# Performance work log

Measured on AMD Instinct MI355X. Metric: run time of the kernel, lower is better.

Reference implementation:

```python
import jax, jax.numpy as jnp
import numpy as np

N = 50000
E = 800000
F = 128
HID = 128
C = 40
GAMMA = 0.1
EPS = 0.1


def gcn(x, theta, src, dst, n):
    # GCNConv (bias=False) with added self-loops and symmetric normalization.
    xw = x @ theta  # [N, d]
    ones = jnp.ones(src.shape[0], dtype=x.dtype)
    deg = jax.ops.segment_sum(ones, dst, num_segments=n) + 1.0  # in-degree incl. self loop
    dinv = jax.lax.rsqrt(deg)
    norm = dinv[src] * dinv[dst]            # [E]
    msg = xw[src] * norm[:, None]           # [E, d]  (dominant memory traffic)
    agg = jax.ops.segment_sum(msg, dst, num_segments=n)
    return agg + xw * (dinv * dinv)[:, None]  # self-loop contribution


def antisym_conv(x, W, bias, theta, src, dst, n):
    # PyG AntiSymmetricConv, num_iters=1, act=tanh, eps=0.1, gamma=0.1
    M = W - W.T - GAMMA * jnp.eye(W.shape[0], dtype=x.dtype)
    h = gcn(x, theta, src, dst, n)
    h = x @ M.T + h + bias
    return x + EPS * jnp.tanh(h)


def setup_inputs() -> dict:
    key = jax.random.key(0)
    ks = jax.random.split(key, 12)
    s = 0.05
    return {
        "x": jax.random.normal(ks[0], (N, F), dtype=jnp.float32),
        "edge_index": jax.random.randint(ks[1], (2, E), 0, N, dtype=jnp.int64)
        if jax.config.jax_enable_x64 else jax.random.randint(ks[1], (2, E), 0, N, dtype=jnp.int32),
        # AntiSymmetricConv 1 (num_features channels)
        "W1": jax.random.normal(ks[2], (F, F), dtype=jnp.float32) * s,
        "b1": jnp.zeros((F,), dtype=jnp.float32),
        "T1": jax.random.normal(ks[3], (F, F), dtype=jnp.float32) * s,
        # AntiSymmetricConv 2 (nhid channels)
        "W2": jax.random.normal(ks[4], (HID, HID), dtype=jnp.float32) * s,
        "b2": jnp.zeros((HID,), dtype=jnp.float32),
        "T2": jax.random.normal(ks[5], (HID, HID), dtype=jnp.float32) * s,
        # Linear layers (torch convention: weight [out, in])
        "lw1": jax.random.normal(ks[6], (HID, F), dtype=jnp.float32) * s,
        "lb1": jnp.zeros((HID,), dtype=jnp.float32),
        "lw2": jax.random.normal(ks[7], (C, HID), dtype=jnp.float32) * s,
        "lb2": jnp.zeros((C,), dtype=jnp.float32),
    }


def reference(x, edge_index, W1, b1, T1, W2, b2, T2, lw1, lb1, lw2, lb2):
    src, dst = edge_index[0], edge_index[1]
    n = x.shape[0]
    # eval mode: dropout is identity
    h = antisym_conv(x, W1, b1, T1, src, dst, n)
    h = jax.nn.relu(h)
    h = h @ lw1.T + lb1
    h = jax.nn.relu(h)
    h = antisym_conv(h, W2, b2, T2, src, dst, n)
    h = jax.nn.relu(h)
    x1 = h
    logits = h @ lw2.T + lb2
    result = jax.nn.log_softmax(logits, axis=-1)
    return (result, x1)
```

## Files before the change

kernel.cpp:

```cpp
#include <hip/hip_runtime.h>
#include <hip/hip_bf16.h>
#include <math.h>

#define GAMMA_ 0.1f
#define EPS_ 0.1f
constexpr int BLK = 256;

typedef __attribute__((ext_vector_type(8))) short short8;
typedef __attribute__((ext_vector_type(4))) float f32x4;
typedef __attribute__((ext_vector_type(2))) float f32x2v;
typedef unsigned char u8;

__device__ inline float bflo(uint u) { union { uint i; float f; } v; v.i = u << 16; return v.f; }
__device__ inline float bfhi(uint u) { union { uint i; float f; } v; v.i = u & 0xffff0000u; return v.f; }
__device__ inline ushort f2bf(float f) {
  union { float f; uint i; } v; v.f = f;
  uint i = v.i;
  return (ushort)((i + 0x7fffu + ((i >> 16) & 1u)) >> 16);
}

#if __has_builtin(__builtin_amdgcn_cvt_pk_f32_fp8) && __has_builtin(__builtin_amdgcn_cvt_pk_fp8_f32)
#define HW_FP8 1
#endif

__device__ inline f32x2v fp8x2_dec_sw(uint raw) {
  f32x2v r;
#pragma unroll
  for (int i = 0; i < 2; ++i) {
    uint b = (raw >> (8 * i)) & 0xffu;
    uint em = b & 0x7fu;
    union { uint u; float f; } o;
    o.u = ((b & 0x80u) << 24) | (0x3C000000u + (em << 20));
    r[i] = (em >= 8u) ? o.f : 0.f;
  }
  return r;
}

__device__ inline f32x2v fp8x2_dec(uint raw) {
#ifdef HW_FP8
  return __builtin_amdgcn_cvt_pk_f32_fp8(raw, false);
#else
  return fp8x2_dec_sw(raw);
#endif
}

__device__ inline uint fp8enc1(float x) {
  union { float f; uint u; } v; v.f = x;
  uint s = (v.u >> 24) & 0x80u;
  uint a = v.u & 0x7fffffffu;
  if (a >= 0x43E00000u) return s | 0x7Eu;
  uint r = a + 0x7FFFFu + ((a >> 20) & 1u);
  if (r < 0x3D800000u) return s;
  return s | (((r - 0x3C000000u) >> 20) & 0x7fu);
}

template<bool HI>
__device__ inline uint fp8x2_enc(float f0, float f1, uint old) {
#ifdef HW_FP8
  return __builtin_amdgcn_cvt_pk_fp8_f32(f0, f1, old, HI);
#else
  uint p = fp8enc1(f0) | (fp8enc1(f1) << 8);
  return HI ? ((old & 0x0000ffffu) | (p << 16)) : ((old & 0xffff0000u) | p);
#endif
}

__global__ void k_count(const int* __restrict__ dst, int* cnt,
                        int* __restrict__ rank, int e) {
  int i = blockIdx.x * BLK + threadIdx.x;
  if (i < e) rank[i] = atomicAdd(&cnt[dst[i]], 1);
}

__global__ void k_scan1(const int* __restrict__ cnt, int* __restrict__ rowp,
                        int* __restrict__ bsum, int n) {
  __shared__ int s[BLK];
  int t = threadIdx.x;
  int i = blockIdx.x * BLK + t;
  int v = (i < n) ? cnt[i] : 0;
  s[t] = v; __syncthreads();
  for (int off = 1; off < BLK; off <<= 1) {
    int u = (t >= off) ? s[t - off] : 0;
    __syncthreads();
    s[t] += u;
    __syncthreads();
  }
  if (i < n) rowp[i] = s[t] - v;
  if (t == BLK - 1) bsum[blockIdx.x] = s[t];
}

__global__ void k_scan2(const int* __restrict__ bsum, int* __restrict__ boff, int nb) {
  __shared__ int s[BLK];
  int t = threadIdx.x;
  int v = (t < nb) ? bsum[t] : 0;
  s[t] = v; __syncthreads();
  for (int off = 1; off < BLK; off <<= 1) {
    int u = (t >= off) ? s[t - off] : 0;
    __syncthreads();
    s[t] += u;
    __syncthreads();
  }
  if (t < nb) boff[t] = s[t] - v;
}

__global__ void k_scan3(const int* __restrict__ boff, int* __restrict__ rowp,
                        const int* __restrict__ cnt, float* __restrict__ dinv,
                        int n, int e) {
  int i = blockIdx.x * BLK + threadIdx.x;
  if (i < n) {
    rowp[i] += boff[blockIdx.x];
    dinv[i] = rsqrtf((float)cnt[i] + 1.0f);
    if (i == 0) rowp[n] = e;
  }
}

__global__ void k_fill(const int* __restrict__ src, const int* __restrict__ dst,
                       const int* __restrict__ rowp, const int* __restrict__ rank,
                       int* __restrict__ csrc, int e) {
  int i = blockIdx.x * BLK + threadIdx.x;
  if (i < e) {
    int d = dst[i];
    csrc[rowp[d] + rank[i]] = src[i];
  }
}

__global__ void k_pack(const float* __restrict__ W1, const float* __restrict__ T1,
                       const float* __restrict__ W2, const float* __restrict__ T2,
                       const float* __restrict__ lw1, const float* __restrict__ lw2,
                       ushort* __restrict__ Bpk1, ushort* __restrict__ Bpk2,
                       ushort* __restrict__ Bpkl, ushort* __restrict__ Bpk2l) {
  int idx = blockIdx.x * BLK + threadIdx.x;
  if (idx < 65536) {
    int which = idx >> 15;
    int e = idx & 32767;
    int k = e >> 8, c = e & 255;
    const float* W = which ? W2 : W1;
    const float* T = which ? T2 : T1;
    float v;
    if (c < 128) {
      v = T[k * 128 + c];
    } else {
      int cc = c - 128;
      v = W[cc * 128 + k] - W[k * 128 + cc] - ((cc == k) ? GAMMA_ : 0.f);
    }
    int kt = k >> 5, q = (k >> 3) & 3, j = k & 7;
    ushort* B = which ? Bpk2 : Bpk1;
    B[(((kt * 4 + q) * 256 + c) << 3) + j] = f2bf(v);
  } else if (idx < 81920) {
    int e = idx - 65536;
    int k = e >> 7, c = e & 127;
    float v = lw1[c * 128 + k];
    int kt = k >> 5, q = (k >> 3) & 3, j = k & 7;
    Bpkl[(((kt * 4 + q) * 128 + c) << 3) + j] = f2bf(v);
  } else {
    int e = idx - 81920;
    if (e < 6144) {
      int k = e / 48, c = e - k * 48;
      float v = (c < 40) ? lw2[c * 128 + k] : 0.f;
      int kt = k >> 5, q = (k >> 3) & 3, j = k & 7;
      Bpk2l[(((kt * 4 + q) * 48 + c) << 3) + j] = f2bf(v);
    }
  }
}

template<bool FP32A>
__global__ __launch_bounds__(256) void k_mgemm(
    const void* __restrict__ Av, int nrows,
    const ushort* __restrict__ Bpk, const float* __restrict__ dinv,
    ushort* __restrict__ O1, u8* __restrict__ Oq) {
  __shared__ ushort S[64 * 256];
  const int t = threadIdx.x;
  const int w = t >> 6, l = t & 63;
  const int lr = l & 15, lq = l >> 4;
  const int r0 = blockIdx.x * 64;
#pragma unroll
  for (int it = 0; it < 4; ++it) {
    int chunk = it * 256 + t;
    int row = chunk >> 4, c16 = chunk & 15;
    int gr = min(r0 + row, nrows - 1);
    ushort* p = S + row * 128 + (c16 ^ (row & 7)) * 8;
    if (FP32A) {
      const float* A = (const float*)Av + (size_t)gr * 128 + c16 * 8;
      float4 v0 = *(const float4*)(A);
      float4 v1 = *(const float4*)(A + 4);
      ushort4 o0 = {f2bf(v0.x), f2bf(v0.y), f2bf(v0.z), f2bf(v0.w)};
      ushort4 o1 = {f2bf(v1.x), f2bf(v1.y), f2bf(v1.z), f2bf(v1.w)};
      *(ushort4*)(p) = o0;
      *(ushort4*)(p + 4) = o1;
    } else {
      const ushort* A = (const ushort*)Av + (size_t)gr * 128 + c16 * 8;
      *(uint4*)p = *(const uint4*)A;
    }
  }
  __syncthreads();
  f32x4 acc[4][4];
#pragma unroll
  for (int rt = 0; rt < 4; ++rt)
#pragma unroll
    for (int n = 0; n < 4; ++n) acc[rt][n] = f32x4{0.f, 0.f, 0.f, 0.f};
#pragma unroll
  for (int kt = 0; kt < 4; ++kt) {
    short8 af[4];
#pragma unroll
    for (int rt = 0; rt < 4; ++rt) {
      int row = rt * 16 + lr;
      af[rt] = *(const short8*)(S + row * 128 + ((kt * 4 + lq) ^ (row & 7)) * 8);
    }
    const ushort* bbase = Bpk + ((size_t)((kt * 4 + lq) * 256) + w * 64 + lr) * 8;
#pragma unroll
    for (int n = 0; n < 4; ++n) {
      short8 bf = *(const short8*)(bbase + n * 16 * 8);
#pragma unroll
      for (int rt = 0; rt < 4; ++rt)
        acc[rt][n] = __builtin_amdgcn_mfma_f32_16x16x32_bf16(af[rt], bf, acc[rt][n], 0, 0, 0);
    }
  }
  __syncthreads();
#pragma unroll
  for (int rt = 0; rt < 4; ++rt)
#pragma unroll
    for (int n = 0; n < 4; ++n)
#pragma unroll
      for (int r = 0; r < 4; ++r) {
        int row = rt * 16 + lq * 4 + r;
        int col = w * 64 + n * 16 + lr;
        int pcol = col ^ (((row >> 2) & 3) << 3);
        S[row * 256 + pcol] = f2bf(acc[rt][n][r]);
      }
  __syncthreads();
#pragma unroll
  for (int it = 0; it < 4; ++it) {
    int idx = it * 256 + t;
    int row = idx >> 4, c8 = idx & 15;
    if (r0 + row < nrows) {
      int pc = (16 + (c8 ^ ((row >> 2) & 3))) * 8;
      uint4 v = *(const uint4*)(S + row * 256 + pc);
      *(uint4*)(O1 + (size_t)(r0 + row) * 128 + c8 * 8) = v;
    }
  }
#pragma unroll
  for (int it = 0; it < 4; ++it) {
    int idx = it * 256 + t;
    int row = idx >> 4, c8 = idx & 15;
    if (r0 + row < nrows) {
      float di = dinv[r0 + row];
      int pc = (c8 ^ ((row >> 2) & 3)) * 8;
      const uint* p = (const uint*)(S + row * 256 + pc);
      uint u0 = p[0], u1 = p[1], u2 = p[2], u3 = p[3];
      uint lo = fp8x2_enc<false>(bflo(u0) * di, bfhi(u0) * di, 0u);
      lo = fp8x2_enc<true>(bflo(u1) * di, bfhi(u1) * di, lo);
      uint hi = fp8x2_enc<false>(bflo(u2) * di, bfhi(u2) * di, 0u);
      hi = fp8x2_enc<true>(bflo(u3) * di, bfhi(u3) * di, hi);
      uint2 ov = { lo, hi };
      *(uint2*)(Oq + (size_t)(r0 + row) * 128 + c8 * 8) = ov;
    }
  }
}

__device__ inline void gather_node(const u8* __restrict__ xq,
                                   const int* __restrict__ csrc,
                                   int e0, int e1, int l, int node,
                                   float& a0, float& a1) {
  uint su = *(const ushort*)(xq + (size_t)node * 128 + 2 * l);
  f32x2v sf = fp8x2_dec(su);
  a0 = sf[0]; a1 = sf[1];
  int e = e0;
  for (; e + 15 < e1; e += 16) {
    int s[16];
#pragma unroll
    for (int u = 0; u < 16; ++u) s[u] = csrc[e + u];
    uint g[16];
#pragma unroll
    for (int u = 0; u < 16; ++u)
      g[u] = *(const ushort*)(xq + (size_t)s[u] * 128 + 2 * l);
#pragma unroll
    for (int u = 0; u < 16; ++u) {
      f32x2v f = fp8x2_dec(g[u]);
      a0 += f[0]; a1 += f[1];
    }
  }
  if (e + 7 < e1) {
    int s[8];
#pragma unroll
    for (int u = 0; u < 8; ++u) s[u] = csrc[e + u];
    uint g[8];
#pragma unroll
    for (int u = 0; u < 8; ++u)
      g[u] = *(const ushort*)(xq + (size_t)s[u] * 128 + 2 * l);
#pragma unroll
    for (int u = 0; u < 8; ++u) {
      f32x2v f = fp8x2_dec(g[u]);
      a0 += f[0]; a1 += f[1];
    }
    e += 8;
  }
  if (e + 3 < e1) {
    int s[4];
#pragma unroll
    for (int u = 0; u < 4; ++u) s[u] = csrc[e + u];
    uint g[4];
#pragma unroll
    for (int u = 0; u < 4; ++u)
      g[u] = *(const ushort*)(xq + (size_t)s[u] * 128 + 2 * l);
#pragma unroll
    for (int u = 0; u < 4; ++u) {
      f32x2v f = fp8x2_dec(g[u]);
      a0 += f[0]; a1 += f[1];
    }
    e += 4;
  }
  for (; e < e1; ++e) {
    uint g0 = *(const ushort*)(xq + (size_t)csrc[e] * 128 + 2 * l);
    f32x2v f = fp8x2_dec(g0);
    a0 += f[0]; a1 += f[1];
  }
}

__global__ __launch_bounds__(512) void k_aggl(
    const u8* __restrict__ xq, const ushort* __restrict__ xmb,
    const float* __restrict__ xinf, const float* __restrict__ dinv,
    const int* __restrict__ rowp, const int* __restrict__ csrc,
    const float* __restrict__ bias, const ushort* __restrict__ Bpkl,
    const float* __restrict__ lb1, ushort* __restrict__ h2b, int n) {
  __shared__ ushort Hs[32 * 128];
  const int t = threadIdx.x;
  const int w = t >> 6, l = t & 63;
  const int lr = l & 15, lq = l >> 4;
  const int r0 = blockIdx.x * 32;
#pragma unroll
  for (int i = 0; i < 4; ++i) {
    int lrow = w * 4 + i;
    int node = r0 + lrow;
    float o0 = 0.f, o1 = 0.f;
    if (node < n) {
      float a0, a1;
      gather_node(xq, csrc, rowp[node], rowp[node + 1], l, node, a0, a1);
      float di = dinv[node];
      uint mu = *(const uint*)(xmb + (size_t)node * 128 + 2 * l);
      float h0 = a0 * di + bflo(mu) + bias[2 * l];
      float h1 = a1 * di + bfhi(mu) + bias[2 * l + 1];
      float2 xv = *(const float2*)(xinf + (size_t)node * 128 + 2 * l);
      o0 = fmaxf(xv.x + EPS_ * tanhf(h0), 0.f);
      o1 = fmaxf(xv.y + EPS_ * tanhf(h1), 0.f);
    }
    ushort2 o = { f2bf(o0), f2bf(o1) };
    *(ushort2*)(Hs + lrow * 128 + ((l >> 2) ^ (lrow & 7)) * 8 + (l & 3) * 2) = o;
  }
  __syncthreads();
  f32x4 acc[2];
  acc[0] = f32x4{0.f, 0.f, 0.f, 0.f};
  acc[1] = f32x4{0.f, 0.f, 0.f, 0.f};
#pragma unroll
  for (int kt = 0; kt < 4; ++kt) {
    short8 bf = *(const short8*)(Bpkl + ((size_t)((kt * 4 + lq) * 128) + w * 16 + lr) * 8);
#pragma unroll
    for (int rt = 0; rt < 2; ++rt) {
      int row = rt * 16 + lr;
      short8 af = *(const short8*)(Hs + row * 128 + ((kt * 4 + lq) ^ (row & 7)) * 8);
      acc[rt] = __builtin_amdgcn_mfma_f32_16x16x32_bf16(af, bf, acc[rt], 0, 0, 0);
    }
  }
  int col = w * 16 + lr;
  float bv = lb1[col];
#pragma unroll
  for (int rt = 0; rt < 2; ++rt)
#pragma unroll
    for (int r = 0; r < 4; ++r) {
      int row = rt * 16 + lq * 4 + r;
      if (r0 + row < n)
        h2b[(size_t)(r0 + row) * 128 + col] = f2bf(fmaxf(acc[rt][r] + bv, 0.f));
    }
}

__global__ __launch_bounds__(256) void k_aggc(
    const u8* __restrict__ xq, const ushort* __restrict__ xmb,
    const ushort* __restrict__ xinb, const float* __restrict__ dinv,
    const int* __restrict__ rowp, const int* __restrict__ csrc,
    const float* __restrict__ bias, float* __restrict__ outf, int n) {
  int node = blockIdx.x * 4 + (threadIdx.x >> 6);
  if (node >= n) return;
  int l = threadIdx.x & 63;
  float a0, a1;
  gather_node(xq, csrc, rowp[node], rowp[node + 1], l, node, a0, a1);
  float di = dinv[node];
  uint mu = *(const uint*)(xmb + (size_t)node * 128 + 2 * l);
  float h0 = a0 * di + bflo(mu) + bias[2 * l];
  float h1 = a1 * di + bfhi(mu) + bias[2 * l + 1];
  uint xu = *(const uint*)(xinb + (size_t)node * 128 + 2 * l);
  float o0 = fmaxf(bflo(xu) + EPS_ * tanhf(h0), 0.f);
  float o1 = fmaxf(bfhi(xu) + EPS_ * tanhf(h1), 0.f);
  float2 o = { o0, o1 };
  *(float2*)(outf + (size_t)node * 128 + 2 * l) = o;
}

__global__ __launch_bounds__(256) void k_logits2(
    const float* __restrict__ X, const ushort* __restrict__ Bpk,
    const float* __restrict__ lb2, float* __restrict__ out, int n) {
  __shared__ float Ls[64 * 49];
  __shared__ float bl[48];
  const int t = threadIdx.x;
  if (t < 48) bl[t] = (t < 40) ? lb2[t] : 0.f;
  const int w = t >> 6, l = t & 63;
  const int lr = l & 15, lq = l >> 4;
  const int r0 = blockIdx.x * 64;
  const int ar = min(r0 + w * 16 + lr, n - 1);
  const float* Ap = X + (size_t)ar * 128 + lq * 8;
  f32x4 acc[3];
#pragma unroll
  for (int nn = 0; nn < 3; ++nn) acc[nn] = f32x4{0.f, 0.f, 0.f, 0.f};
#pragma unroll
  for (int kt = 0; kt < 4; ++kt) {
    float4 xa = *(const float4*)(Ap + kt * 32);
    float4 xc = *(const float4*)(Ap + kt * 32 + 4);
    short8 af;
    af[0] = (short)f2bf(xa.x); af[1] = (short)f2bf(xa.y);
    af[2] = (short)f2bf(xa.z); af[3] = (short)f2bf(xa.w);
    af[4] = (short)f2bf(xc.x); af[5] = (short)f2bf(xc.y);
    af[6] = (short)f2bf(xc.z); af[7] = (short)f2bf(xc.w);
    const ushort* bbase = Bpk + ((size_t)((kt * 4 + lq) * 48) + lr) * 8;
#pragma unroll
    for (int nn = 0; nn < 3; ++nn) {
      short8 bf = *(const short8*)(bbase + nn * 16 * 8);
      acc[nn] = __builtin_amdgcn_mfma_f32_16x16x32_bf16(af, bf, acc[nn], 0, 0, 0);
    }
  }
  __syncthreads();
#pragma unroll
  for (int nn = 0; nn < 3; ++nn)
#pragma unroll
    for (int r = 0; r < 4; ++r) {
      int row = w * 16 + lq * 4 + r;
      int col = nn * 16 + lr;
      Ls[row * 49 + col] = acc[nn][r] + bl[col];
    }
  __syncthreads();
  int row = t >> 2, q = t & 3;
  if (r0 + row >= n) return;
  const float* Lr = Ls + row * 49 + q * 10;
  float m = -1e30f;
#pragma unroll
  for (int c = 0; c < 10; ++c) m = fmaxf(m, Lr[c]);
  m = fmaxf(m, __shfl_xor(m, 1));
  m = fmaxf(m, __shfl_xor(m, 2));
  float s = 0.f;
#pragma unroll
  for (int c = 0; c < 10; ++c) s += expf(Lr[c] - m);
  s += __shfl_xor(s, 1);
  s += __shfl_xor(s, 2);
  float lse = m + logf(s);
  float* Or = out + (size_t)(r0 + row) * 40 + q * 10;
#pragma unroll
  for (int c = 0; c < 10; ++c) Or[c] = Lr[c] - lse;
}

extern "C" void kernel_launch(void* const* d_in, const int* in_sizes, int n_in,
                              void* d_out, int out_size, void* d_ws, size_t ws_size,
                              hipStream_t stream) {
  const float* x   = (const float*)d_in[0];
  const int*   ei  = (const int*)d_in[1];
  const float* W1  = (const float*)d_in[2];
  const float* b1  = (const float*)d_in[3];
  const float* T1  = (const float*)d_in[4];
  const float* W2  = (const float*)d_in[5];
  const float* b2  = (const float*)d_in[6];
  const float* T2  = (const float*)d_in[7];
  const float* lw1 = (const float*)d_in[8];
  const float* lb1 = (const float*)d_in[9];
  const float* lw2 = (const float*)d_in[10];
  const float* lb2 = (const float*)d_in[11];
  const int N = in_sizes[0] / 128;
  const int E = in_sizes[1] / 2;
  const int* src = ei;
  const int* dst = ei + E;

  float* ws = (float*)d_ws;
  size_t o = 0;
  float* dinv = ws;             o += N;
  int* cnt = (int*)(ws + o);    o += N;
  int* rowp = (int*)(ws + o);   o += (size_t)(N + 4);
  int* csrc = (int*)(ws + o);   o += E;
  int* rank = (int*)(ws + o);   o += E;
  int* bsum = (int*)(ws + o);   o += 256;
  int* boff = (int*)(ws + o);   o += 256;
  o = (o + 3) & ~(size_t)3;
  ushort* us = (ushort*)(ws + o);
  size_t uo = 0;
  ushort* Bpk1 = us + uo;       uo += 32768;
  ushort* Bpk2 = us + uo;       uo += 32768;
  ushort* Bpkl = us + uo;       uo += 16384;
  ushort* Bpk2l = us + uo;      uo += 6144;
  ushort* xmb  = us + uo;       uo += (size_t)N * 128;
  ushort* h2b  = us + uo;       uo += (size_t)N * 128;
  u8* xq = (u8*)(us + uo);

  float* outp = (float*)d_out;
  float* x1 = outp + (size_t)N * 40;

  int nb_n = (N + BLK - 1) / BLK;
  int nb_e = (E + BLK - 1) / BLK;
  int nb_r = (N + 63) / 64;

  hipMemsetAsync(cnt, 0, (size_t)N * sizeof(int), stream);
  k_count<<<nb_e, BLK, 0, stream>>>(dst, cnt, rank, E);
  k_scan1<<<nb_n, BLK, 0, stream>>>(cnt, rowp, bsum, N);
  k_scan2<<<1, BLK, 0, stream>>>(bsum, boff, nb_n);
  k_scan3<<<nb_n, BLK, 0, stream>>>(boff, rowp, cnt, dinv, N, E);
  k_fill<<<nb_e, BLK, 0, stream>>>(src, dst, rowp, rank, csrc, E);
  k_pack<<<344, BLK, 0, stream>>>(W1, T1, W2, T2, lw1, lw2, Bpk1, Bpk2, Bpkl, Bpk2l);

  k_mgemm<true><<<nb_r, 256, 0, stream>>>(x, N, Bpk1, dinv, xmb, xq);
  k_aggl<<<(N + 31) / 32, 512, 0, stream>>>(
      xq, xmb, x, dinv, rowp, csrc, b1, Bpkl, lb1, h2b, N);
  k_mgemm<false><<<nb_r, 256, 0, stream>>>(h2b, N, Bpk2, dinv, xmb, xq);
  k_aggc<<<(N + 3) / 4, 256, 0, stream>>>(
      xq, xmb, h2b, dinv, rowp, csrc, b2, x1, N);
  k_logits2<<<(N + 63) / 64, 256, 0, stream>>>(x1, Bpk2l, lb2, outp, N);
}
```

Measured before the change: 194.3 us.

## Fuse second-layer projection GEMM into the aggregation+linear kernel

The second AntiSymmetricConv's combined GEMM (h2 @ [M2|T2]), along with its fp8 quantization scaled by dinv, now runs inside k_aggl. It uses the h2 tile already held in shared memory, so the separate k_mgemm launch and its re-read of h2b from global memory go away. New buffers xmb2 and xq2 keep the outputs from aliasing the first layer's xmb and xq, which k_aggl is still reading. The gather loop also drops its 16-wide unroll in favour of an 8-wide loop, which should lower register pressure in the now larger kernel. The extra work per block and the larger shared memory use could reduce occupancy in the gather-bound phase.

```diff
diff --git a/kernel.cpp b/kernel.cpp
--- a/kernel.cpp
+++ b/kernel.cpp
@@ -161,9 +161,8 @@
   }
 }
 
-template<bool FP32A>
 __global__ __launch_bounds__(256) void k_mgemm(
-    const void* __restrict__ Av, int nrows,
+    const float* __restrict__ Av, int nrows,
     const ushort* __restrict__ Bpk, const float* __restrict__ dinv,
     ushort* __restrict__ O1, u8* __restrict__ Oq) {
   __shared__ ushort S[64 * 256];
@@ -177,18 +176,13 @@
     int row = chunk >> 4, c16 = chunk & 15;
     int gr = min(r0 + row, nrows - 1);
     ushort* p = S + row * 128 + (c16 ^ (row & 7)) * 8;
-    if (FP32A) {
-      const float* A = (const float*)Av + (size_t)gr * 128 + c16 * 8;
-      float4 v0 = *(const float4*)(A);
-      float4 v1 = *(const float4*)(A + 4);
-      ushort4 o0 = {f2bf(v0.x), f2bf(v0.y), f2bf(v0.z), f2bf(v0.w)};
-      ushort4 o1 = {f2bf(v1.x), f2bf(v1.y), f2bf(v1.z), f2bf(v1.w)};
-      *(ushort4*)(p) = o0;
-      *(ushort4*)(p + 4) = o1;
-    } else {
-      const ushort* A = (const ushort*)Av + (size_t)gr * 128 + c16 * 8;
-      *(uint4*)p = *(const uint4*)A;
-    }
+    const float* A = Av + (size_t)gr * 128 + c16 * 8;
+    float4 v0 = *(const float4*)(A);
+    float4 v1 = *(const float4*)(A + 4);
+    ushort4 o0 = {f2bf(v0.x), f2bf(v0.y), f2bf(v0.z), f2bf(v0.w)};
+    ushort4 o1 = {f2bf(v1.x), f2bf(v1.y), f2bf(v1.z), f2bf(v1.w)};
+    *(ushort4*)(p) = o0;
+    *(ushort4*)(p + 4) = o1;
   }
   __syncthreads();
   f32x4 acc[4][4];
@@ -263,21 +257,7 @@
   f32x2v sf = fp8x2_dec(su);
   a0 = sf[0]; a1 = sf[1];
   int e = e0;
-  for (; e + 15 < e1; e += 16) {
-    int s[16];
-#pragma unroll
-    for (int u = 0; u < 16; ++u) s[u] = csrc[e + u];
-    uint g[16];
-#pragma unroll
-    for (int u = 0; u < 16; ++u)
-      g[u] = *(const ushort*)(xq + (size_t)s[u] * 128 + 2 * l);
-#pragma unroll
-    for (int u = 0; u < 16; ++u) {
-      f32x2v f = fp8x2_dec(g[u]);
-      a0 += f[0]; a1 += f[1];
-    }
-  }
-  if (e + 7 < e1) {
+  for (; e + 7 < e1; e += 8) {
     int s[8];
 #pragma unroll
     for (int u = 0; u < 8; ++u) s[u] = csrc[e + u];
@@ -290,7 +270,6 @@
       f32x2v f = fp8x2_dec(g[u]);
       a0 += f[0]; a1 += f[1];
     }
-    e += 8;
   }
   if (e + 3 < e1) {
     int s[4];
@@ -319,8 +298,12 @@
     const float* __restrict__ xinf, const float* __restrict__ dinv,
     const int* __restrict__ rowp, const int* __restrict__ csrc,
     const float* __restrict__ bias, const ushort* __restrict__ Bpkl,
-    const float* __restrict__ lb1, ushort* __restrict__ h2b, int n) {
-  __shared__ ushort Hs[32 * 128];
+    const float* __restrict__ lb1, const ushort* __restrict__ Bpk2,
+    ushort* __restrict__ h2b, ushort* __restrict__ xmb2, u8* __restrict__ xq2,
+    int n) {
+  __shared__ ushort S[32 * 256];
+  ushort* Sa = S;
+  ushort* Sb = S + 32 * 128;
   const int t = threadIdx.x;
   const int w = t >> 6, l = t & 63;
   const int lr = l & 15, lq = l >> 4;
@@ -342,7 +325,7 @@
       o1 = fmaxf(xv.y + EPS_ * tanhf(h1), 0.f);
     }
     ushort2 o = { f2bf(o0), f2bf(o1) };
-    *(ushort2*)(Hs + lrow * 128 + ((l >> 2) ^ (lrow & 7)) * 8 + (l & 3) * 2) = o;
+    *(ushort2*)(Sa + lrow * 128 + ((l >> 2) ^ (lrow & 7)) * 8 + (l & 3) * 2) = o;
   }
   __syncthreads();
   f32x4 acc[2];
@@ -354,20 +337,78 @@
 #pragma unroll
     for (int rt = 0; rt < 2; ++rt) {
       int row = rt * 16 + lr;
-      short8 af = *(const short8*)(Hs + row * 128 + ((kt * 4 + lq) ^ (row & 7)) * 8);
+      short8 af = *(const short8*)(Sa + row * 128 + ((kt * 4 + lq) ^ (row & 7)) * 8);
       acc[rt] = __builtin_amdgcn_mfma_f32_16x16x32_bf16(af, bf, acc[rt], 0, 0, 0);
     }
   }
-  int col = w * 16 + lr;
-  float bv = lb1[col];
+  {
+    int col = w * 16 + lr;
+    float bv = lb1[col];
+#pragma unroll
+    for (int rt = 0; rt < 2; ++rt)
+#pragma unroll
+      for (int r = 0; r < 4; ++r) {
+        int row = rt * 16 + lq * 4 + r;
+        ushort hb = f2bf(fmaxf(acc[rt][r] + bv, 0.f));
+        if (r0 + row < n)
+          h2b[(size_t)(r0 + row) * 128 + col] = hb;
+        Sb[row * 128 + ((col >> 3) ^ (row & 7)) * 8 + (col & 7)] = hb;
+      }
+  }
+  __syncthreads();
+  f32x4 acc2[2][2];
 #pragma unroll
   for (int rt = 0; rt < 2; ++rt)
 #pragma unroll
-    for (int r = 0; r < 4; ++r) {
-      int row = rt * 16 + lq * 4 + r;
-      if (r0 + row < n)
-        h2b[(size_t)(r0 + row) * 128 + col] = f2bf(fmaxf(acc[rt][r] + bv, 0.f));
-    }
+    for (int ct = 0; ct < 2; ++ct) acc2[rt][ct] = f32x4{0.f, 0.f, 0.f, 0.f};
+#pragma unroll
+  for (int kt = 0; kt < 4; ++kt) {
+    short8 af[2];
+#pragma unroll
+    for (int rt = 0; rt < 2; ++rt) {
+      int row = rt * 16 + lr;
+      af[rt] = *(const short8*)(Sb + row * 128 + ((kt * 4 + lq) ^ (row & 7)) * 8);
+    }
+#pragma unroll
+    for (int ct = 0; ct < 2; ++ct) {
+      const ushort* bb = Bpk2 + ((size_t)((kt * 4 + lq) * 256) + w * 32 + ct * 16 + lr) * 8;
+      short8 bf = *(const short8*)bb;
+#pragma unroll
+      for (int rt = 0; rt < 2; ++rt)
+        acc2[rt][ct] = __builtin_amdgcn_mfma_f32_16x16x32_bf16(af[rt], bf, acc2[rt][ct], 0, 0, 0);
+    }
+  }
+  __syncthreads();
+#pragma unroll
+  for (int rt = 0; rt < 2; ++rt)
+#pragma unroll
+    for (int ct = 0; ct < 2; ++ct)
+#pragma unroll
+      for (int r = 0; r < 4; ++r) {
+        int row = rt * 16 + lq * 4 + r;
+        int col = w * 32 + ct * 16 + lr;
+        int pcol = col ^ (((row >> 2) & 3) << 3);
+        S[row * 256 + pcol] = f2bf(acc2[rt][ct][r]);
+      }
+  __syncthreads();
+  {
+    int row = t >> 4, c8 = t & 15;
+    if (r0 + row < n) {
+      int pc = (16 + (c8 ^ ((row >> 2) & 3))) * 8;
+      uint4 v = *(const uint4*)(S + row * 256 + pc);
+      *(uint4*)(xmb2 + (size_t)(r0 + row) * 128 + c8 * 8) = v;
+      float di = dinv[r0 + row];
+      int pq = (c8 ^ ((row >> 2) & 3)) * 8;
+      const uint* p = (const uint*)(S + row * 256 + pq);
+      uint u0 = p[0], u1 = p[1], u2 = p[2], u3 = p[3];
+      uint lo = fp8x2_enc<false>(bflo(u0) * di, bfhi(u0) * di, 0u);
+      lo = fp8x2_enc<true>(bflo(u1) * di, bfhi(u1) * di, lo);
+      uint hi = fp8x2_enc<false>(bflo(u2) * di, bfhi(u2) * di, 0u);
+      hi = fp8x2_enc<true>(bflo(u3) * di, bfhi(u3) * di, hi);
+      uint2 ov = { lo, hi };
+      *(uint2*)(xq2 + (size_t)(r0 + row) * 128 + c8 * 8) = ov;
+    }
+  }
 }
 
 __global__ __launch_bounds__(256) void k_aggc(
@@ -488,8 +529,10 @@
   ushort* Bpkl = us + uo;       uo += 16384;
   ushort* Bpk2l = us + uo;      uo += 6144;
   ushort* xmb  = us + uo;       uo += (size_t)N * 128;
+  ushort* xmb2 = us + uo;       uo += (size_t)N * 128;
   ushort* h2b  = us + uo;       uo += (size_t)N * 128;
-  u8* xq = (u8*)(us + uo);
+  u8* xq  = (u8*)(us + uo);     uo += (size_t)N * 64;
+  u8* xq2 = (u8*)(us + uo);
 
   float* outp = (float*)d_out;
   float* x1 = outp + (size_t)N * 40;
@@ -506,11 +549,10 @@
   k_fill<<<nb_e, BLK, 0, stream>>>(src, dst, rowp, rank, csrc, E);
   k_pack<<<344, BLK, 0, stream>>>(W1, T1, W2, T2, lw1, lw2, Bpk1, Bpk2, Bpkl, Bpk2l);
 
-  k_mgemm<true><<<nb_r, 256, 0, stream>>>(x, N, Bpk1, dinv, xmb, xq);
+  k_mgemm<<<nb_r, 256, 0, stream>>>(x, N, Bpk1, dinv, xmb, xq);
   k_aggl<<<(N + 31) / 32, 512, 0, stream>>>(
-      xq, xmb, x, dinv, rowp, csrc, b1, Bpkl, lb1, h2b, N);
-  k_mgemm<false><<<nb_r, 256, 0, stream>>>(h2b, N, Bpk2, dinv, xmb, xq);
+      xq, xmb, x, dinv, rowp, csrc, b1, Bpkl, lb1, Bpk2, h2b, xmb2, xq2, N);
   k_aggc<<<(N + 3) / 4, 256, 0, stream>>>(
-      xq, xmb, h2b, dinv, rowp, csrc, b2, x1, N);
+      xq2, xmb2, h2b, dinv, rowp, csrc, b2, x1, N);
   k_logits2<<<(N + 63) / 64, 256, 0, stream>>>(x1, Bpk2l, lb2, outp, N);
 }
```

Measured after the change: 174.0 us. 1.12x faster.
